# Kernel tuning notes

Measured on AMD Instinct MI355X. Metric: run time of the kernel, lower is better.

Reference implementation:

```python
import jax, jax.numpy as jnp
import numpy as np

B, S, D_IN = 1, 1024, 2048
H_QK, H_V, DK, DV = 8, 16, 128, 128
KCONV = 4
D_OUT = H_QK * DK          # 1024
D_OUT_VG = H_V * DV        # 2048
FUSED = 2 * D_OUT + D_OUT_VG  # 4096
EPS = 1e-6


def setup_inputs() -> dict:
    key = jax.random.key(0)
    ks = jax.random.split(key, 8)
    return {
        "x": jax.random.normal(ks[0], (B, S, D_IN), jnp.float32),
        "w_qkv": jax.random.normal(ks[1], (FUSED, D_IN), jnp.float32) * 0.02,
        "w_gate": jax.random.normal(ks[2], (D_OUT_VG, D_IN), jnp.float32) * 0.02,
        "w_beta": jax.random.normal(ks[3], (H_V, D_IN), jnp.float32) * 0.02,
        "w_alpha": jax.random.normal(ks[4], (H_V, D_IN), jnp.float32) * 0.02,
        "log_A": jnp.log(jax.random.uniform(ks[5], (H_V,), jnp.float32, 1e-3, 16.0)),
        "dt_bias": jnp.ones((H_V,), jnp.float32),
        "conv_w": jax.random.normal(ks[6], (FUSED, 1, KCONV), jnp.float32) * 0.1,
        "rms_w": jnp.ones((DV,), jnp.float32),
        "w_out": jax.random.normal(ks[7], (D_IN, D_OUT_VG), jnp.float32) * 0.02,
    }


def l2_norm(t):
    return t / jnp.sqrt(jnp.sum(t * t, axis=-1, keepdims=True) + EPS)


def rms_norm(t, w):
    var = jnp.mean(t * t, axis=-1, keepdims=True)
    return t * jax.lax.rsqrt(var + EPS) * w


def gated_delta_rule(q, k, v, beta, alpha):
    # q,k: (b,h,s,dk)  v: (b,h,s,dv)  beta,alpha: (b,h,s)
    q = q * (q.shape[-1] ** -0.5)
    S0 = jnp.zeros(q.shape[:2] + (q.shape[-1], v.shape[-1]), q.dtype)

    def step(Sm, inp):
        q_t, k_t, v_t, b_t, a_t = inp  # (b,h,dk) (b,h,dk) (b,h,dv) (b,h) (b,h)
        Sm = Sm * a_t[..., None, None]                      # decay state
        kv = jnp.einsum('bhk,bhkv->bhv', k_t, Sm)           # k^T S
        u = (v_t - kv) * b_t[..., None]                     # delta-rule target
        Sm = Sm + k_t[..., None] * u[:, :, None, :]         # rank-1 update
        o = jnp.einsum('bhk,bhkv->bhv', q_t, Sm)
        return Sm, o

    xs = (jnp.moveaxis(q, 2, 0), jnp.moveaxis(k, 2, 0), jnp.moveaxis(v, 2, 0),
          jnp.moveaxis(beta, 2, 0), jnp.moveaxis(alpha, 2, 0))
    Sf, outs = jax.lax.scan(step, S0, xs)
    return jnp.moveaxis(outs, 0, 2), Sf  # (b,h,s,dv)


def reference(x, w_qkv, w_gate, w_beta, w_alpha, log_A, dt_bias, conv_w, rms_w, w_out):
    b, seq_len, _ = x.shape
    fused_qkv = x @ w_qkv.T                                  # (b,s,FUSED)
    beta = jax.nn.sigmoid(x @ w_beta.T).transpose(0, 2, 1)   # (b,h_v,s)
    token_projs = x @ w_alpha.T                              # (b,s,h_v)
    alpha = jnp.exp(-jnp.exp(log_A) * jax.nn.softplus(token_projs + dt_bias))
    alpha = alpha.transpose(0, 2, 1)                         # (b,h_v,s)

    # causal depthwise conv1d (padding k-1, truncate to seq_len) + SiLU
    conv_in = fused_qkv.transpose(0, 2, 1)                   # (b,C,s)
    conv_out = jax.lax.conv_general_dilated(
        conv_in, conv_w, window_strides=(1,), padding=[(KCONV - 1, 0)],
        dimension_numbers=('NCH', 'OIH', 'NCH'), feature_group_count=FUSED)
    fused_qkv = jax.nn.silu(conv_out).transpose(0, 2, 1)     # (b,s,C)

    query = fused_qkv[..., :D_OUT].reshape(b, seq_len, H_QK, DK).transpose(0, 2, 1, 3)
    key = fused_qkv[..., D_OUT:2 * D_OUT].reshape(b, seq_len, H_QK, DK).transpose(0, 2, 1, 3)
    value = fused_qkv[..., 2 * D_OUT:].reshape(b, seq_len, H_V, DV).transpose(0, 2, 1, 3)

    query, key = l2_norm(query), l2_norm(key)
    rep = H_V // H_QK
    if rep > 1:
        query = jnp.repeat(query, rep, axis=1)
        key = jnp.repeat(key, rep, axis=1)

    ctx, _ = gated_delta_rule(query, key, value, beta, alpha)  # (b,h_v,s,dv)
    ctx = rms_norm(ctx.astype(jnp.float32), rms_w)
    ctx = ctx.transpose(0, 2, 1, 3).reshape(b, seq_len, D_OUT_VG)

    gate = jax.nn.silu(x @ w_gate.T)
    return (gate * ctx) @ w_out.T
```

## Files before the change

kernel.cpp:

```cpp
#include <hip/hip_runtime.h>

#define AS1 __attribute__((address_space(1)))
#define AS3 __attribute__((address_space(3)))

typedef _Float16 f16x8 __attribute__((ext_vector_type(8)));
typedef _Float16 f16x4 __attribute__((ext_vector_type(4)));
typedef _Float16 f16x2 __attribute__((ext_vector_type(2)));
typedef float f32x4 __attribute__((ext_vector_type(4)));

#define MFMA16(a, b, c) __builtin_amdgcn_mfma_f32_16x16x32_f16((a), (b), (c), 0, 0, 0)

__device__ __forceinline__ float silu_f(float v) { return v / (1.f + expf(-v)); }

__device__ __forceinline__ void gload_lds16(const void* g, void* l) {
    __builtin_amdgcn_global_load_lds((AS1 void*)g, (AS3 void*)l, 16, 0, 0);
}

__global__ __launch_bounds__(256) void cvt_proj(const float* __restrict__ x,
                                                const float* __restrict__ w_qkv,
                                                const float* __restrict__ w_gate,
                                                const float* __restrict__ w_out,
                                                _Float16* __restrict__ dst,
                                                const float* __restrict__ w_beta,
                                                const float* __restrict__ w_alpha,
                                                const float* __restrict__ log_A,
                                                const float* __restrict__ dt_bias,
                                                float* __restrict__ betaB,
                                                float* __restrict__ lalphaB) {
    __shared__ float xs[2048];
    const int bid = blockIdx.x, tid = threadIdx.x;
    if (bid < 18432) {
        long i = ((long)bid * 256 + tid) * 4;
        const float* src; long off;
        if (i < 2097152)       { src = x;      off = 0; }
        else if (i < 10485760) { src = w_qkv;  off = 2097152; }
        else if (i < 14680064) { src = w_gate; off = 10485760; }
        else                   { src = w_out;  off = 14680064; }
        float4 v = *(const float4*)&src[i - off];
        f16x4 h = { (_Float16)v.x, (_Float16)v.y, (_Float16)v.z, (_Float16)v.w };
        *(f16x4*)&dst[i] = h;
        return;
    }
    const int s = bid - 18432;
    *(float4*)&xs[tid * 8]     = *(const float4*)&x[(long)s * 2048 + tid * 8];
    *(float4*)&xs[tid * 8 + 4] = *(const float4*)&x[(long)s * 2048 + tid * 8 + 4];
    __syncthreads();
    const int o = tid >> 3, j = tid & 7;
    const float* w = (o < 16) ? &w_beta[(long)o * 2048] : &w_alpha[(long)(o - 16) * 2048];
    float p = 0.f;
#pragma unroll 4
    for (int i = 0; i < 64; i++) {
        int d = i * 32 + j * 4;
        float4 wv = *(const float4*)&w[d];
        p += xs[d] * wv.x + xs[d + 1] * wv.y + xs[d + 2] * wv.z + xs[d + 3] * wv.w;
    }
    p += __shfl_xor(p, 1); p += __shfl_xor(p, 2); p += __shfl_xor(p, 4);
    if (j == 0) {
        if (o < 16) {
            betaB[s * 16 + o] = 1.f / (1.f + expf(-p));
        } else {
            int h = o - 16;
            float t = p + dt_bias[h];
            float sp = (t > 20.f) ? t : log1pf(expf(t));
            lalphaB[s * 16 + h] = -expf(log_A[h]) * sp;
        }
    }
}

__global__ __launch_bounds__(256) void gemm_bt64h(const _Float16* __restrict__ A,
                                                  const _Float16* __restrict__ B,
                                                  _Float16* __restrict__ C, int N, int K) {
    __shared__ _Float16 S[192 * 32];
    const int tid = threadIdx.x;
    const int rowA0 = blockIdx.y * 64, rowB0 = blockIdx.x * 128;
    const int lane = tid & 63;
    const int wv = tid >> 6;
    const int rw = (wv & 1) * 32, cw = (wv >> 1) * 64;
    const int fr = lane & 15, kof = (lane >> 4) * 8;

    const _Float16* gp[3];
#pragma unroll
    for (int i = 0; i < 3; i++) {
        int u = tid + 256 * i;
        int row = u >> 2, c0 = (u & 3) * 8;
        gp[i] = (row < 64) ? A + (long)(rowA0 + row) * K + c0
                           : B + (long)(rowB0 + row - 64) * K + c0;
    }

    f32x4 zero = {0.f, 0.f, 0.f, 0.f};
    f32x4 acc[2][4];
#pragma unroll
    for (int mi = 0; mi < 2; mi++)
#pragma unroll
        for (int ni = 0; ni < 4; ni++) acc[mi][ni] = zero;

    for (int k0 = 0; k0 < K; k0 += 32) {
        __syncthreads();
#pragma unroll
        for (int i = 0; i < 3; i++)
            gload_lds16(gp[i] + k0, &S[(tid + 256 * i) * 8]);
        __syncthreads();
        f16x8 af[2], bf[4];
#pragma unroll
        for (int mi = 0; mi < 2; mi++) af[mi] = *(const f16x8*)&S[(rw + mi * 16 + fr) * 32 + kof];
#pragma unroll
        for (int ni = 0; ni < 4; ni++) bf[ni] = *(const f16x8*)&S[(64 + cw + ni * 16 + fr) * 32 + kof];
#pragma unroll
        for (int mi = 0; mi < 2; mi++)
#pragma unroll
            for (int ni = 0; ni < 4; ni++)
                acc[mi][ni] = MFMA16(af[mi], bf[ni], acc[mi][ni]);
    }
    const int rbase = (lane >> 4) * 4;
#pragma unroll
    for (int mi = 0; mi < 2; mi++)
#pragma unroll
        for (int ni = 0; ni < 4; ni++) {
            int row = rowA0 + rw + mi * 16 + rbase;
            int col = rowB0 + cw + ni * 16 + fr;
#pragma unroll
            for (int r = 0; r < 4; r++)
                C[(long)(row + r) * N + col] = (_Float16)acc[mi][ni][r];
        }
}

__global__ __launch_bounds__(256) void gemm_bt6464(const _Float16* __restrict__ A,
                                                   const _Float16* __restrict__ B,
                                                   float* __restrict__ C, int N, int K) {
    __shared__ _Float16 S[128 * 32];
    const int tid = threadIdx.x;
    const int rowA0 = blockIdx.y * 64, rowB0 = blockIdx.x * 64;
    const int lane = tid & 63;
    const int wv = tid >> 6;
    const int rw = (wv & 1) * 32, cwol = (wv >> 1) * 32;
    const int fr = lane & 15, kof = (lane >> 4) * 8;

    const _Float16* gp[2];
#pragma unroll
    for (int i = 0; i < 2; i++) {
        int u = tid + 256 * i;
        int row = u >> 2, c0 = (u & 3) * 8;
        gp[i] = (row < 64) ? A + (long)(rowA0 + row) * K + c0
                           : B + (long)(rowB0 + row - 64) * K + c0;
    }

    f32x4 zero = {0.f, 0.f, 0.f, 0.f};
    f32x4 acc[2][2];
#pragma unroll
    for (int mi = 0; mi < 2; mi++)
#pragma unroll
        for (int ni = 0; ni < 2; ni++) acc[mi][ni] = zero;

    for (int k0 = 0; k0 < K; k0 += 32) {
        __syncthreads();
#pragma unroll
        for (int i = 0; i < 2; i++)
            gload_lds16(gp[i] + k0, &S[(tid + 256 * i) * 8]);
        __syncthreads();
        f16x8 af[2], bf[2];
#pragma unroll
        for (int mi = 0; mi < 2; mi++) af[mi] = *(const f16x8*)&S[(rw + mi * 16 + fr) * 32 + kof];
#pragma unroll
        for (int ni = 0; ni < 2; ni++) bf[ni] = *(const f16x8*)&S[(64 + cwol + ni * 16 + fr) * 32 + kof];
#pragma unroll
        for (int mi = 0; mi < 2; mi++)
#pragma unroll
            for (int ni = 0; ni < 2; ni++)
                acc[mi][ni] = MFMA16(af[mi], bf[ni], acc[mi][ni]);
    }
    const int rbase = (lane >> 4) * 4;
#pragma unroll
    for (int mi = 0; mi < 2; mi++)
#pragma unroll
        for (int ni = 0; ni < 2; ni++) {
            int row = rowA0 + rw + mi * 16 + rbase;
            int col = rowB0 + cwol + ni * 16 + fr;
#pragma unroll
            for (int r = 0; r < 4; r++)
                C[(long)(row + r) * N + col] = acc[mi][ni][r];
        }
}

__global__ __launch_bounds__(512) void chunk_front(const _Float16* __restrict__ pre,
                                                   const float* __restrict__ cw,
                                                   const float* __restrict__ betaB,
                                                   const float* __restrict__ lalphaB,
                                                   _Float16* __restrict__ Mw,
                                                   _Float16* __restrict__ QTw,
                                                   _Float16* __restrict__ KTw,
                                                   _Float16* __restrict__ WTw,
                                                   _Float16* __restrict__ Bw,
                                                   _Float16* __restrict__ BTw,
                                                   float* __restrict__ gamC) {
    __shared__ _Float16 Kh[64 * 136];
    __shared__ _Float16 Qh[64 * 136];
    __shared__ _Float16 Vh[64 * 136];
    __shared__ _Float16 Tl[64 * 72];
    __shared__ float lg[64], betL[64], bgamL[64], egQ[64], egKr[64];
    const int hc = blockIdx.x, h = hc >> 4, c = hc & 15, hq = h >> 1, s0 = c * 64;
    const int tid = threadIdx.x;

    if (tid < 64) {
        float la = lalphaB[(s0 + tid) * 16 + h];
#pragma unroll
        for (int d = 1; d < 64; d <<= 1) {
            float tv = __shfl_up(la, d, 64);
            if (tid >= d) la += tv;
        }
        lg[tid] = la;
        float la63 = __shfl(la, 63, 64);
        float b = betaB[(s0 + tid) * 16 + h];
        float eg = expf(la);
        betL[tid] = b;
        bgamL[tid] = b * eg;
        egQ[tid] = eg;
        egKr[tid] = expf(la63 - la);
        if (tid == 63) gamC[hc] = eg;
    }

    {
        const int tt = tid >> 3, pp = tid & 7, m0 = pp * 16;
        const _Float16* rp[4];
        bool ok0, ok1, ok2;
        {
            int sb = s0 + tt - 3;
            ok0 = (sb >= 0); ok1 = (sb + 1 >= 0); ok2 = (sb + 2 >= 0);
            rp[0] = pre + (long)sb * 6144;
            rp[1] = pre + (long)(sb + 1) * 6144;
            rp[2] = pre + (long)(sb + 2) * 6144;
            rp[3] = pre + (long)(sb + 3) * 6144;
        }
#pragma unroll
        for (int sel = 0; sel < 3; sel++) {
            const int colbase = (sel == 0) ? hq * 128 : (sel == 1) ? 1024 + hq * 128
                                                                   : 2048 + h * 128;
            float vals[16];
            float ss = 0.f;
#pragma unroll
            for (int g = 0; g < 2; g++) {
                const int co = colbase + m0 + g * 8;
                f16x8 r0 = {}, r1 = {}, r2 = {}, r3;
                if (ok0) r0 = *(const f16x8*)&rp[0][co];
                if (ok1) r1 = *(const f16x8*)&rp[1][co];
                if (ok2) r2 = *(const f16x8*)&rp[2][co];
                r3 = *(const f16x8*)&rp[3][co];
#pragma unroll
                for (int j = 0; j < 8; j++) {
                    float4 w = *(const float4*)&cw[(co + j) * 4];
                    float a = (float)r0[j] * w.x + (float)r1[j] * w.y +
                              (float)r2[j] * w.z + (float)r3[j] * w.w;
                    a = silu_f(a);
                    vals[g * 8 + j] = a;
                    ss += a * a;
                }
            }
            float sc = 1.f;
            if (sel < 2) {
                ss += __shfl_xor(ss, 1); ss += __shfl_xor(ss, 2); ss += __shfl_xor(ss, 4);
                sc = rsqrtf(ss + 1e-6f);
                if (sel == 0) sc *= 0.08838834764831843f;
            }
            _Float16* dst = (sel == 0) ? Qh : (sel == 1) ? Kh : Vh;
#pragma unroll
            for (int g = 0; g < 2; g++) {
                f16x8 hv;
#pragma unroll
                for (int j = 0; j < 8; j++) hv[j] = (_Float16)(vals[g * 8 + j] * sc);
                *(f16x8*)&dst[tt * 136 + m0 + g * 8] = hv;
            }
        }
    }
    __syncthreads();

    const int wv = tid >> 6, lane = tid & 63;
    const int fr = lane & 15, kof = (lane >> 4) * 8, quad = lane >> 4;
    {
        f32x4 zero = {0.f, 0.f, 0.f, 0.f};
        if (wv < 4) {
            f32x4 accT[4];
#pragma unroll
            for (int ci = 0; ci < 4; ci++) accT[ci] = zero;
            for (int k0 = 0; k0 < 128; k0 += 32) {
                f16x8 ak = *(const f16x8*)&Kh[(wv * 16 + fr) * 136 + k0 + kof];
#pragma unroll
                for (int ci = 0; ci < 4; ci++)
                    accT[ci] = MFMA16(ak, *(const f16x8*)&Kh[(ci * 16 + fr) * 136 + k0 + kof], accT[ci]);
            }
#pragma unroll
            for (int ci = 0; ci < 4; ci++)
#pragma unroll
                for (int r = 0; r < 4; r++) {
                    int t = wv * 16 + quad * 4 + r, i = ci * 16 + fr;
                    float e = expf(lg[t] - lg[i]);
                    Tl[t * 72 + i] = (_Float16)((i < t) ? betL[t] * e * accT[ci][r] : 0.f);
                }
        } else {
            const int w = wv - 4;
            f32x4 accM[4];
#pragma unroll
            for (int ci = 0; ci < 4; ci++) accM[ci] = zero;
            for (int k0 = 0; k0 < 128; k0 += 32) {
                f16x8 aq = *(const f16x8*)&Qh[(w * 16 + fr) * 136 + k0 + kof];
#pragma unroll
                for (int ci = 0; ci < 4; ci++)
                    accM[ci] = MFMA16(aq, *(const f16x8*)&Kh[(ci * 16 + fr) * 136 + k0 + kof], accM[ci]);
            }
#pragma unroll
            for (int ci = 0; ci < 4; ci++)
#pragma unroll
                for (int r = 0; r < 4; r++) {
                    int t = w * 16 + quad * 4 + r, i = ci * 16 + fr;
                    float e = expf(lg[t] - lg[i]);
                    Mw[(long)hc * 4096 + t * 64 + i] = (_Float16)((i <= t) ? e * accM[ci][r] : 0.f);
                }
        }
    }
    __syncthreads();

    if (wv < 4) {
        const int jcol = tid & 127;
        const _Float16* Xsrc = (wv < 2) ? Vh : Kh;
        const float* dscale = (wv < 2) ? betL : bgamL;
        float Xs[64];
#pragma unroll
        for (int t = 0; t < 64; t++) Xs[t] = dscale[t] * (float)Xsrc[t * 136 + jcol];
#pragma unroll
        for (int a = 0; a < 4; a++) {
#pragma unroll
            for (int b = 0; b < a; b++) {
#pragma unroll
                for (int r = 0; r < 16; r++) {
                    const _Float16* trow = &Tl[(a * 16 + r) * 72 + b * 16];
                    f16x8 t0 = *(const f16x8*)trow;
                    f16x8 t1 = *(const f16x8*)(trow + 8);
                    float acc = 0.f;
#pragma unroll
                    for (int k = 0; k < 8; k++) acc += (float)t0[k] * Xs[b * 16 + k];
#pragma unroll
                    for (int k = 0; k < 8; k++) acc += (float)t1[k] * Xs[b * 16 + 8 + k];
                    Xs[a * 16 + r] -= acc;
                }
            }
#pragma unroll
            for (int sp = 1; sp < 16; sp++) {
                const _Float16* trow = &Tl[(a * 16 + sp) * 72 + a * 16];
                f16x8 t0 = *(const f16x8*)trow;
                f16x8 t1 = *(const f16x8*)(trow + 8);
                float acc = 0.f;
#pragma unroll
                for (int tp = 0; tp < 16; tp++) {
                    if (tp < sp) acc += (float)(tp < 8 ? t0[tp] : t1[tp - 8]) * Xs[a * 16 + tp];
                }
                Xs[a * 16 + sp] -= acc;
            }
        }
        if (wv < 2) {
#pragma unroll
            for (int v = 0; v < 8; v++) {
                f16x8 hv;
#pragma unroll
                for (int j = 0; j < 8; j++) hv[j] = (_Float16)Xs[v * 8 + j];
                *(f16x8*)&WTw[((long)hc * 128 + jcol) * 64 + v * 8] = hv;
            }
        } else {
#pragma unroll
            for (int t = 0; t < 64; t++) Bw[(long)hc * 8192 + t * 128 + jcol] = (_Float16)Xs[t];
#pragma unroll
            for (int v = 0; v < 8; v++) {
                f16x8 hv;
#pragma unroll
                for (int j = 0; j < 8; j++) hv[j] = (_Float16)Xs[v * 8 + j];
                *(f16x8*)&BTw[((long)hc * 128 + jcol) * 64 + v * 8] = hv;
            }
        }
    } else {
        const int w = wv - 4;
#pragma unroll
        for (int cp = 0; cp < 4; cp++) {
            int t = w * 16 + fr;
            int cc = cp * 32 + kof;
            f16x8 q = *(const f16x8*)&Qh[t * 136 + cc];
            float s = egQ[t];
            f16x8 o;
#pragma unroll
            for (int j = 0; j < 8; j++) o[j] = (_Float16)(s * (float)q[j]);
            *(f16x8*)&QTw[(long)hc * 8192 + t * 128 + cc] = o;
        }
        const int m = w * 32 + (lane & 31);
        const int tb = (lane >> 5) * 8;
#pragma unroll
        for (int tp = 0; tp < 4; tp++) {
            int t0 = tb + tp * 16;
            f16x8 o;
#pragma unroll
            for (int j = 0; j < 8; j++)
                o[j] = (_Float16)(egKr[t0 + j] * (float)Kh[(t0 + j) * 136 + m]);
            *(f16x8*)&KTw[(long)hc * 8192 + m * 64 + t0] = o;
        }
    }
}

__global__ __launch_bounds__(256) void gr_kernel(const _Float16* __restrict__ KTw,
                                                 const _Float16* __restrict__ BTw,
                                                 const _Float16* __restrict__ WTw,
                                                 _Float16* __restrict__ Gw,
                                                 float* __restrict__ Rtw) {
    __shared__ _Float16 KTl[128 * 72], BTl[128 * 72], WTl[128 * 72];
    const long hc = blockIdx.x;
    const int tid = threadIdx.x;
    {
        int r = tid >> 1, c0 = (tid & 1) * 32;
        const _Float16* k_ = &KTw[hc * 8192 + r * 64 + c0];
        const _Float16* b_ = &BTw[hc * 8192 + r * 64 + c0];
        const _Float16* w_ = &WTw[hc * 8192 + r * 64 + c0];
#pragma unroll
        for (int i = 0; i < 4; i++) {
            *(f16x8*)&KTl[r * 72 + c0 + i * 8] = *(const f16x8*)&k_[i * 8];
            *(f16x8*)&BTl[r * 72 + c0 + i * 8] = *(const f16x8*)&b_[i * 8];
            *(f16x8*)&WTl[r * 72 + c0 + i * 8] = *(const f16x8*)&w_[i * 8];
        }
    }
    __syncthreads();
    const int wv = tid >> 6, lane = tid & 63;
    const int fr = lane & 15, kof = (lane >> 4) * 8, quad = lane >> 4;
    f32x4 zero = {0.f, 0.f, 0.f, 0.f};
#pragma unroll
    for (int mi = 0; mi < 2; mi++) {
        int m0 = (wv * 2 + mi) * 16;
        f16x8 a0 = *(const f16x8*)&KTl[(m0 + fr) * 72 + kof];
        f16x8 a1 = *(const f16x8*)&KTl[(m0 + fr) * 72 + 32 + kof];
#pragma unroll
        for (int nj = 0; nj < 8; nj++) {
            f32x4 acc = zero;
            acc = MFMA16(a0, *(const f16x8*)&BTl[(nj * 16 + fr) * 72 + kof], acc);
            acc = MFMA16(a1, *(const f16x8*)&BTl[(nj * 16 + fr) * 72 + 32 + kof], acc);
#pragma unroll
            for (int r = 0; r < 4; r++)
                Gw[hc * 16384 + (long)(m0 + quad * 4 + r) * 128 + nj * 16 + fr] = (_Float16)acc[r];
        }
    }
#pragma unroll
    for (int ji = 0; ji < 2; ji++) {
        int j0 = (wv * 2 + ji) * 16;
        f16x8 a0 = *(const f16x8*)&WTl[(j0 + fr) * 72 + kof];
        f16x8 a1 = *(const f16x8*)&WTl[(j0 + fr) * 72 + 32 + kof];
#pragma unroll
        for (int nm = 0; nm < 8; nm++) {
            f32x4 acc = zero;
            acc = MFMA16(a0, *(const f16x8*)&KTl[(nm * 16 + fr) * 72 + kof], acc);
            acc = MFMA16(a1, *(const f16x8*)&KTl[(nm * 16 + fr) * 72 + 32 + kof], acc);
#pragma unroll
            for (int r = 0; r < 4; r++)
                Rtw[hc * 16384 + (long)(j0 + quad * 4 + r) * 128 + nm * 16 + fr] = acc[r];
        }
    }
}

__global__ __launch_bounds__(256) void serial_scan(const _Float16* __restrict__ Gw,
                                                   const float* __restrict__ Rtw,
                                                   const float* __restrict__ gamC,
                                                   float* __restrict__ Zdump) {
    __shared__ _Float16 Zhi[32 * 136], Zlo[32 * 136];
    __shared__ _Float16 Gl[128 * 136];
    const int tid = threadIdx.x;
    const int h = blockIdx.x >> 2, js = (blockIdx.x & 3) * 32;
    const int wv = tid >> 6, lane = tid & 63;
    const int fr = lane & 15, kof = (lane >> 4) * 8, quad = lane >> 4;
    const int gr_ = tid >> 1, gc_ = (tid & 1) * 64;

    for (int e = tid; e < 32 * 136; e += 256) { Zhi[e] = (_Float16)0.f; Zlo[e] = (_Float16)0.f; }
    float z[2][2][4];
#pragma unroll
    for (int jt = 0; jt < 2; jt++)
#pragma unroll
        for (int u = 0; u < 2; u++)
#pragma unroll
            for (int r = 0; r < 4; r++) z[jt][u][r] = 0.f;

    long hc0 = (long)h * 16;
    f16x8 gpre[8];
#pragma unroll
    for (int i = 0; i < 8; i++)
        gpre[i] = *(const f16x8*)&Gw[hc0 * 16384 + (long)gr_ * 128 + gc_ + i * 8];
    float rpre[2][2][4];
#pragma unroll
    for (int jt = 0; jt < 2; jt++)
#pragma unroll
        for (int u = 0; u < 2; u++)
#pragma unroll
            for (int r = 0; r < 4; r++)
                rpre[jt][u][r] = Rtw[hc0 * 16384 +
                                     (long)(js + jt * 16 + quad * 4 + r) * 128 +
                                     (2 * wv + u) * 16 + fr];
    __syncthreads();

    for (int c = 0; c < 16; ++c) {
        long hc = (long)h * 16 + c;
        float gC = gamC[hc];
#pragma unroll
        for (int i = 0; i < 8; i++)
            *(f16x8*)&Gl[gr_ * 136 + gc_ + i * 8] = gpre[i];
        long hcn = (long)h * 16 + (c < 15 ? c + 1 : 15);
        f16x8 gnext[8];
#pragma unroll
        for (int i = 0; i < 8; i++)
            gnext[i] = *(const f16x8*)&Gw[hcn * 16384 + (long)gr_ * 128 + gc_ + i * 8];
        float rnext[2][2][4];
#pragma unroll
        for (int jt = 0; jt < 2; jt++)
#pragma unroll
            for (int u = 0; u < 2; u++)
#pragma unroll
                for (int r = 0; r < 4; r++)
                    rnext[jt][u][r] = Rtw[hcn * 16384 +
                                          (long)(js + jt * 16 + quad * 4 + r) * 128 +
                                          (2 * wv + u) * 16 + fr];
        __syncthreads();
        f32x4 acc[2][2];
        f32x4 zero = {0.f, 0.f, 0.f, 0.f};
#pragma unroll
        for (int jt = 0; jt < 2; jt++)
#pragma unroll
            for (int u = 0; u < 2; u++) acc[jt][u] = zero;
        for (int k0 = 0; k0 < 128; k0 += 32) {
            f16x8 ahi[2], alo[2], bfr[2];
#pragma unroll
            for (int jt = 0; jt < 2; jt++) {
                ahi[jt] = *(const f16x8*)&Zhi[(jt * 16 + fr) * 136 + k0 + kof];
                alo[jt] = *(const f16x8*)&Zlo[(jt * 16 + fr) * 136 + k0 + kof];
            }
#pragma unroll
            for (int u = 0; u < 2; u++)
                bfr[u] = *(const f16x8*)&Gl[((2 * wv + u) * 16 + fr) * 136 + k0 + kof];
#pragma unroll
            for (int jt = 0; jt < 2; jt++)
#pragma unroll
                for (int u = 0; u < 2; u++) {
                    acc[jt][u] = MFMA16(ahi[jt], bfr[u], acc[jt][u]);
                    acc[jt][u] = MFMA16(alo[jt], bfr[u], acc[jt][u]);
                }
        }
        __syncthreads();
#pragma unroll
        for (int jt = 0; jt < 2; jt++)
#pragma unroll
            for (int u = 0; u < 2; u++)
#pragma unroll
                for (int r = 0; r < 4; r++) {
                    int j = jt * 16 + quad * 4 + r;
                    int m = (2 * wv + u) * 16 + fr;
                    Zdump[hc * 16384 + (long)(js + j) * 128 + m] = z[jt][u][r];
                    float zn = gC * z[jt][u][r] - acc[jt][u][r] + rpre[jt][u][r];
                    z[jt][u][r] = zn;
                    _Float16 hi = (_Float16)zn;
                    Zhi[j * 136 + m] = hi;
                    Zlo[j * 136 + m] = (_Float16)(zn - (float)hi);
                }
#pragma unroll
        for (int i = 0; i < 8; i++) gpre[i] = gnext[i];
#pragma unroll
        for (int jt = 0; jt < 2; jt++)
#pragma unroll
            for (int u = 0; u < 2; u++)
#pragma unroll
                for (int r = 0; r < 4; r++) rpre[jt][u][r] = rnext[jt][u][r];
    }
}

__global__ __launch_bounds__(256) void out_chunk(const float* __restrict__ Zdump,
                                                 const _Float16* __restrict__ Bw,
                                                 const _Float16* __restrict__ WTw,
                                                 const _Float16* __restrict__ QTw,
                                                 const _Float16* __restrict__ Mw,
                                                 float* __restrict__ ctx) {
    __shared__ _Float16 SThi[64 * 136], STlo[64 * 136], Bl[64 * 136];
    __shared__ _Float16 UT[64 * 72];
    const int bid = blockIdx.x;
    const long hc = bid >> 1;
    const int jh = (bid & 1) * 64;
    const int h = (int)(hc >> 4), c = (int)(hc & 15), s0 = c * 64;
    const int tid = threadIdx.x, wv = tid >> 6, lane = tid & 63;
    const int fr = lane & 15, kof = (lane >> 4) * 8, quad = lane >> 4;
    {
        int r = tid >> 2, c0 = (tid & 3) * 32;
        const float* src = &Zdump[hc * 16384 + (long)(jh + r) * 128 + c0];
#pragma unroll
        for (int i = 0; i < 8; i++) {
            float4 v = *(const float4*)&src[i * 4];
            _Float16 h0 = (_Float16)v.x, h1 = (_Float16)v.y, h2 = (_Float16)v.z, h3 = (_Float16)v.w;
            f16x4 hi = {h0, h1, h2, h3};
            f16x4 lo = {(_Float16)(v.x - (float)h0), (_Float16)(v.y - (float)h1),
                        (_Float16)(v.z - (float)h2), (_Float16)(v.w - (float)h3)};
            *(f16x4*)&SThi[r * 136 + c0 + i * 4] = hi;
            *(f16x4*)&STlo[r * 136 + c0 + i * 4] = lo;
        }
        const _Float16* bsrc = &Bw[hc * 8192 + r * 128 + c0];
#pragma unroll
        for (int i = 0; i < 4; i++)
            *(f16x8*)&Bl[r * 136 + c0 + i * 8] = *(const f16x8*)&bsrc[i * 8];
    }
    __syncthreads();
    const int t0 = wv * 16;
    f16x8 ba[4];
#pragma unroll
    for (int k = 0; k < 4; k++)
        ba[k] = *(const f16x8*)&Bl[(t0 + fr) * 136 + k * 32 + kof];
#pragma unroll
    for (int jt = 0; jt < 4; jt++) {
        f32x4 acc = {0.f, 0.f, 0.f, 0.f};
#pragma unroll
        for (int k = 0; k < 4; k++) {
            acc = MFMA16(ba[k], *(const f16x8*)&SThi[(jt * 16 + fr) * 136 + k * 32 + kof], acc);
            acc = MFMA16(ba[k], *(const f16x8*)&STlo[(jt * 16 + fr) * 136 + k * 32 + kof], acc);
        }
#pragma unroll
        for (int r = 0; r < 4; r++) {
            int t = t0 + quad * 4 + r;
            int j = jt * 16 + fr;
            float w = (float)WTw[hc * 8192 + (long)(jh + j) * 64 + t];
            UT[j * 72 + t] = (_Float16)(w - acc[r]);
        }
    }
    __syncthreads();
    f16x8 qa[4], ma[2];
#pragma unroll
    for (int k = 0; k < 4; k++)
        qa[k] = *(const f16x8*)&QTw[hc * 8192 + (long)(t0 + fr) * 128 + k * 32 + kof];
#pragma unroll
    for (int k = 0; k < 2; k++)
        ma[k] = *(const f16x8*)&Mw[hc * 4096 + (long)(t0 + fr) * 64 + k * 32 + kof];
#pragma unroll
    for (int jt = 0; jt < 4; jt++) {
        f32x4 acc = {0.f, 0.f, 0.f, 0.f};
#pragma unroll
        for (int k = 0; k < 4; k++) {
            acc = MFMA16(qa[k], *(const f16x8*)&SThi[(jt * 16 + fr) * 136 + k * 32 + kof], acc);
            acc = MFMA16(qa[k], *(const f16x8*)&STlo[(jt * 16 + fr) * 136 + k * 32 + kof], acc);
        }
#pragma unroll
        for (int k = 0; k < 2; k++)
            acc = MFMA16(ma[k], *(const f16x8*)&UT[(jt * 16 + fr) * 72 + k * 32 + kof], acc);
#pragma unroll
        for (int r = 0; r < 4; r++) {
            int t = t0 + quad * 4 + r;
            int j = jt * 16 + fr;
            ctx[(long)(s0 + t) * 2048 + h * 128 + jh + j] = acc[r];
        }
    }
}

__global__ void epilogue_k(const float* __restrict__ ctx, const _Float16* __restrict__ pre,
                           const float* __restrict__ rms_w, _Float16* __restrict__ y) {
    int gw = (blockIdx.x * blockDim.x + threadIdx.x) >> 6;
    int lane = threadIdx.x & 63;
    int s = gw >> 4, h = gw & 15;
    long base = (long)s * 2048 + h * 128;
    long gbase = (long)s * 6144 + 4096 + h * 128;
    float2 cv = *(const float2*)&ctx[base + lane * 2];
    float ss = cv.x * cv.x + cv.y * cv.y;
#pragma unroll
    for (int m = 1; m < 64; m <<= 1) ss += __shfl_xor(ss, m);
    float sc = rsqrtf(ss * (1.f / 128.f) + 1e-6f);
    int d = lane * 2;
    float2 rw = *(const float2*)&rms_w[d];
    f16x2 gv = *(const f16x2*)&pre[gbase + d];
    float g0 = silu_f((float)gv[0]);
    float g1 = silu_f((float)gv[1]);
    f16x2 hv = { (_Float16)(cv.x * sc * rw.x * g0), (_Float16)(cv.y * sc * rw.y * g1) };
    *(f16x2*)&y[base + d] = hv;
}

extern "C" void kernel_launch(void* const* d_in, const int* in_sizes, int n_in,
                              void* d_out, int out_size, void* d_ws, size_t ws_size,
                              hipStream_t stream) {
    const float* x       = (const float*)d_in[0];
    const float* w_qkv   = (const float*)d_in[1];
    const float* w_gate  = (const float*)d_in[2];
    const float* w_beta  = (const float*)d_in[3];
    const float* w_alpha = (const float*)d_in[4];
    const float* log_A   = (const float*)d_in[5];
    const float* dt_bias = (const float*)d_in[6];
    const float* conv_w  = (const float*)d_in[7];
    const float* rms_w   = (const float*)d_in[8];
    const float* w_out   = (const float*)d_in[9];
    float* outp = (float*)d_out;

    char* ws = (char*)d_ws;
    size_t off = 0;
    _Float16* xb     = (_Float16*)(ws + off); off += (size_t)1024 * 2048 * 2;
    _Float16* wfused = (_Float16*)(ws + off); off += (size_t)6144 * 2048 * 2;
    _Float16* woutb  = (_Float16*)(ws + off); off += (size_t)2048 * 2048 * 2;
    _Float16* yb     = (_Float16*)(ws + off); off += (size_t)1024 * 2048 * 2;
    _Float16* pre    = (_Float16*)(ws + off); off += (size_t)1024 * 6144 * 2;
    float* ctx       = (float*)(ws + off);    off += (size_t)1024 * 16 * 128 * 4;
    float* betaB     = (float*)(ws + off);    off += (size_t)1024 * 16 * 4;
    float* lalphaB   = (float*)(ws + off);    off += (size_t)1024 * 16 * 4;
    _Float16* Mw     = (_Float16*)(ws + off); off += (size_t)256 * 4096 * 2;
    _Float16* QTw    = (_Float16*)(ws + off); off += (size_t)256 * 8192 * 2;
    _Float16* KTw    = (_Float16*)(ws + off); off += (size_t)256 * 8192 * 2;
    _Float16* WTw    = (_Float16*)(ws + off); off += (size_t)256 * 8192 * 2;
    _Float16* Bw     = (_Float16*)(ws + off); off += (size_t)256 * 8192 * 2;
    _Float16* BTw    = (_Float16*)(ws + off); off += (size_t)256 * 8192 * 2;
    float* gamC      = (float*)(ws + off);    off += (size_t)256 * 4;
    _Float16* Gw     = (_Float16*)(ws + off); off += (size_t)256 * 16384 * 2;
    float* Rtw       = (float*)(ws + off);    off += (size_t)256 * 16384 * 4;
    float* Zdump     = (float*)(ws + off);    off += (size_t)256 * 16384 * 4;

    cvt_proj<<<19456, 256, 0, stream>>>(x, w_qkv, w_gate, w_out, xb,
                                        w_beta, w_alpha, log_A, dt_bias, betaB, lalphaB);

    gemm_bt64h<<<dim3(48, 16), 256, 0, stream>>>(xb, wfused, pre, 6144, 2048);

    chunk_front<<<256, 512, 0, stream>>>(pre, conv_w, betaB, lalphaB,
                                         Mw, QTw, KTw, WTw, Bw, BTw, gamC);
    gr_kernel<<<256, 256, 0, stream>>>(KTw, BTw, WTw, Gw, Rtw);
    serial_scan<<<64, 256, 0, stream>>>(Gw, Rtw, gamC, Zdump);
    out_chunk<<<512, 256, 0, stream>>>(Zdump, Bw, WTw, QTw, Mw, ctx);

    epilogue_k<<<4096, 256, 0, stream>>>(ctx, pre, rms_w, yb);
    gemm_bt6464<<<dim3(32, 16), 256, 0, stream>>>(yb, woutb, outp, 2048, 2048);
}
```

Measured before the change: 298.0 us.

## Triple-buffer GEMM LDS loads and enlarge input projection tile to 128x128

Both fp16 GEMMs now use a three-stage LDS ring, issuing global-to-LDS loads two K-tiles ahead and waiting with explicit vmcnt counts plus one barrier per iteration instead of two. This is meant to hide global load latency behind MFMA work. The input projection GEMM also grows from a 64x128 to a 128x128 block tile with 4x4 accumulators per wave, which raises reuse per loaded tile but halves the grid to 384 blocks and increases register and LDS use.

```diff
diff --git a/kernel.cpp b/kernel.cpp
--- a/kernel.cpp
+++ b/kernel.cpp
@@ -67,53 +67,68 @@
     }
 }
 
-__global__ __launch_bounds__(256) void gemm_bt64h(const _Float16* __restrict__ A,
-                                                  const _Float16* __restrict__ B,
-                                                  _Float16* __restrict__ C, int N, int K) {
-    __shared__ _Float16 S[192 * 32];
+__global__ __launch_bounds__(256) void gemm_bt128h(const _Float16* __restrict__ A,
+                                                   const _Float16* __restrict__ B,
+                                                   _Float16* __restrict__ C, int N, int K) {
+    __shared__ _Float16 S[3][256 * 32];
     const int tid = threadIdx.x;
-    const int rowA0 = blockIdx.y * 64, rowB0 = blockIdx.x * 128;
-    const int lane = tid & 63;
-    const int wv = tid >> 6;
-    const int rw = (wv & 1) * 32, cw = (wv >> 1) * 64;
-    const int fr = lane & 15, kof = (lane >> 4) * 8;
-
-    const _Float16* gp[3];
-#pragma unroll
-    for (int i = 0; i < 3; i++) {
-        int u = tid + 256 * i;
-        int row = u >> 2, c0 = (u & 3) * 8;
-        gp[i] = (row < 64) ? A + (long)(rowA0 + row) * K + c0
-                           : B + (long)(rowB0 + row - 64) * K + c0;
-    }
+    const int rowA0 = blockIdx.y * 128, rowB0 = blockIdx.x * 128;
+    const int lane = tid & 63, wv = tid >> 6;
+    const int rw = (wv & 1) * 64, cw = (wv >> 1) * 64;
+    const int fr = lane & 15, kof = (lane >> 4) * 8, quad = lane >> 4;
+
+    const _Float16* gp[4];
+#pragma unroll
+    for (int i = 0; i < 4; i++) {
+        int idx = tid + 256 * i;
+        int row = idx >> 2, c0 = (idx & 3) * 8;
+        gp[i] = (row < 128) ? A + (long)(rowA0 + row) * K + c0
+                            : B + (long)(rowB0 + row - 128) * K + c0;
+    }
+    const int NT = K >> 5;
+
+#pragma unroll
+    for (int i = 0; i < 4; i++) gload_lds16(gp[i], &S[0][(tid + 256 * i) * 8]);
+#pragma unroll
+    for (int i = 0; i < 4; i++) gload_lds16(gp[i] + 32, &S[1][(tid + 256 * i) * 8]);
+    asm volatile("s_waitcnt vmcnt(4)" ::: "memory");
+    __builtin_amdgcn_s_barrier();
 
     f32x4 zero = {0.f, 0.f, 0.f, 0.f};
-    f32x4 acc[2][4];
-#pragma unroll
-    for (int mi = 0; mi < 2; mi++)
+    f32x4 acc[4][4];
+#pragma unroll
+    for (int mi = 0; mi < 4; mi++)
 #pragma unroll
         for (int ni = 0; ni < 4; ni++) acc[mi][ni] = zero;
 
-    for (int k0 = 0; k0 < K; k0 += 32) {
-        __syncthreads();
-#pragma unroll
-        for (int i = 0; i < 3; i++)
-            gload_lds16(gp[i] + k0, &S[(tid + 256 * i) * 8]);
-        __syncthreads();
-        f16x8 af[2], bf[4];
-#pragma unroll
-        for (int mi = 0; mi < 2; mi++) af[mi] = *(const f16x8*)&S[(rw + mi * 16 + fr) * 32 + kof];
-#pragma unroll
-        for (int ni = 0; ni < 4; ni++) bf[ni] = *(const f16x8*)&S[(64 + cw + ni * 16 + fr) * 32 + kof];
-#pragma unroll
-        for (int mi = 0; mi < 2; mi++)
+    int cur = 0;
+    for (int t = 0; t < NT; ++t) {
+        if (t + 2 < NT) {
+            int nb = cur + 2; if (nb >= 3) nb -= 3;
+#pragma unroll
+            for (int i = 0; i < 4; i++)
+                gload_lds16(gp[i] + (t + 2) * 32, &S[nb][(tid + 256 * i) * 8]);
+        }
+        f16x8 af[4], bf[4];
+#pragma unroll
+        for (int mi = 0; mi < 4; mi++)
+            af[mi] = *(const f16x8*)&S[cur][(rw + mi * 16 + fr) * 32 + kof];
+#pragma unroll
+        for (int ni = 0; ni < 4; ni++)
+            bf[ni] = *(const f16x8*)&S[cur][(128 + cw + ni * 16 + fr) * 32 + kof];
+#pragma unroll
+        for (int mi = 0; mi < 4; mi++)
 #pragma unroll
             for (int ni = 0; ni < 4; ni++)
                 acc[mi][ni] = MFMA16(af[mi], bf[ni], acc[mi][ni]);
-    }
-    const int rbase = (lane >> 4) * 4;
-#pragma unroll
-    for (int mi = 0; mi < 2; mi++)
+        if (t + 2 < NT) { asm volatile("s_waitcnt vmcnt(4)" ::: "memory"); }
+        else            { asm volatile("s_waitcnt vmcnt(0)" ::: "memory"); }
+        __builtin_amdgcn_s_barrier();
+        cur = (cur == 2) ? 0 : cur + 1;
+    }
+    const int rbase = quad * 4;
+#pragma unroll
+    for (int mi = 0; mi < 4; mi++)
 #pragma unroll
         for (int ni = 0; ni < 4; ni++) {
             int row = rowA0 + rw + mi * 16 + rbase;
@@ -127,22 +142,29 @@
 __global__ __launch_bounds__(256) void gemm_bt6464(const _Float16* __restrict__ A,
                                                    const _Float16* __restrict__ B,
                                                    float* __restrict__ C, int N, int K) {
-    __shared__ _Float16 S[128 * 32];
+    __shared__ _Float16 S[3][128 * 32];
     const int tid = threadIdx.x;
     const int rowA0 = blockIdx.y * 64, rowB0 = blockIdx.x * 64;
-    const int lane = tid & 63;
-    const int wv = tid >> 6;
+    const int lane = tid & 63, wv = tid >> 6;
     const int rw = (wv & 1) * 32, cwol = (wv >> 1) * 32;
-    const int fr = lane & 15, kof = (lane >> 4) * 8;
+    const int fr = lane & 15, kof = (lane >> 4) * 8, quad = lane >> 4;
 
     const _Float16* gp[2];
 #pragma unroll
     for (int i = 0; i < 2; i++) {
-        int u = tid + 256 * i;
-        int row = u >> 2, c0 = (u & 3) * 8;
+        int idx = tid + 256 * i;
+        int row = idx >> 2, c0 = (idx & 3) * 8;
         gp[i] = (row < 64) ? A + (long)(rowA0 + row) * K + c0
                            : B + (long)(rowB0 + row - 64) * K + c0;
     }
+    const int NT = K >> 5;
+
+#pragma unroll
+    for (int i = 0; i < 2; i++) gload_lds16(gp[i], &S[0][(tid + 256 * i) * 8]);
+#pragma unroll
+    for (int i = 0; i < 2; i++) gload_lds16(gp[i] + 32, &S[1][(tid + 256 * i) * 8]);
+    asm volatile("s_waitcnt vmcnt(2)" ::: "memory");
+    __builtin_amdgcn_s_barrier();
 
     f32x4 zero = {0.f, 0.f, 0.f, 0.f};
     f32x4 acc[2][2];
@@ -151,24 +173,32 @@
 #pragma unroll
         for (int ni = 0; ni < 2; ni++) acc[mi][ni] = zero;
 
-    for (int k0 = 0; k0 < K; k0 += 32) {
-        __syncthreads();
-#pragma unroll
-        for (int i = 0; i < 2; i++)
-            gload_lds16(gp[i] + k0, &S[(tid + 256 * i) * 8]);
-        __syncthreads();
+    int cur = 0;
+    for (int t = 0; t < NT; ++t) {
+        if (t + 2 < NT) {
+            int nb = cur + 2; if (nb >= 3) nb -= 3;
+#pragma unroll
+            for (int i = 0; i < 2; i++)
+                gload_lds16(gp[i] + (t + 2) * 32, &S[nb][(tid + 256 * i) * 8]);
+        }
         f16x8 af[2], bf[2];
 #pragma unroll
-        for (int mi = 0; mi < 2; mi++) af[mi] = *(const f16x8*)&S[(rw + mi * 16 + fr) * 32 + kof];
-#pragma unroll
-        for (int ni = 0; ni < 2; ni++) bf[ni] = *(const f16x8*)&S[(64 + cwol + ni * 16 + fr) * 32 + kof];
+        for (int mi = 0; mi < 2; mi++)
+            af[mi] = *(const f16x8*)&S[cur][(rw + mi * 16 + fr) * 32 + kof];
+#pragma unroll
+        for (int ni = 0; ni < 2; ni++)
+            bf[ni] = *(const f16x8*)&S[cur][(64 + cwol + ni * 16 + fr) * 32 + kof];
 #pragma unroll
         for (int mi = 0; mi < 2; mi++)
 #pragma unroll
             for (int ni = 0; ni < 2; ni++)
                 acc[mi][ni] = MFMA16(af[mi], bf[ni], acc[mi][ni]);
-    }
-    const int rbase = (lane >> 4) * 4;
+        if (t + 2 < NT) { asm volatile("s_waitcnt vmcnt(2)" ::: "memory"); }
+        else            { asm volatile("s_waitcnt vmcnt(0)" ::: "memory"); }
+        __builtin_amdgcn_s_barrier();
+        cur = (cur == 2) ? 0 : cur + 1;
+    }
+    const int rbase = quad * 4;
 #pragma unroll
     for (int mi = 0; mi < 2; mi++)
 #pragma unroll
@@ -709,7 +739,7 @@
     cvt_proj<<<19456, 256, 0, stream>>>(x, w_qkv, w_gate, w_out, xb,
                                         w_beta, w_alpha, log_A, dt_bias, betaB, lalphaB);
 
-    gemm_bt64h<<<dim3(48, 16), 256, 0, stream>>>(xb, wfused, pre, 6144, 2048);
+    gemm_bt128h<<<dim3(48, 8), 256, 0, stream>>>(xb, wfused, pre, 6144, 2048);
 
     chunk_front<<<256, 512, 0, stream>>>(pre, conv_w, betaB, lalphaB,
                                          Mw, QTw, KTw, WTw, Bw, BTw, gamC);
```

Result: faster. 281.5 us (-5.5%).
